# Optimization experiments

Hardware: AMD Instinct MI355X
Metric: run time of the kernel (lower is better)

## Reference

```python
import jax, jax.numpy as jnp
import numpy as np

VOCAB = 50000
EMB = 1024
HID = 1024
H = HID // 2            # per-direction hidden size
NTAG = 34
START = 32
STOP = 33
SEQ = 4096
NEG = -10000.0


def setup_inputs() -> dict:
    key = jax.random.key(0)
    ks = jax.random.split(key, 16)
    s = 0.05

    def rn(k, shape, scale=1.0):
        return (jax.random.normal(k, shape) * scale).astype(jnp.float32)

    logT = jax.random.normal(ks[12], (NTAG, NTAG)).astype(jnp.float32)
    logT = logT.at[START, :].set(NEG).at[:, STOP].set(NEG)
    return {
        "sentence": jax.random.randint(ks[0], (SEQ,), 0, VOCAB),
        "embed": rn(ks[1], (VOCAB, EMB), s),
        "w_ih_f": rn(ks[2], (4 * H, EMB), s), "w_hh_f": rn(ks[3], (4 * H, H), s),
        "b_ih_f": rn(ks[4], (4 * H,), s), "b_hh_f": rn(ks[5], (4 * H,), s),
        "w_ih_b": rn(ks[6], (4 * H, EMB), s), "w_hh_b": rn(ks[7], (4 * H, H), s),
        "b_ih_b": rn(ks[8], (4 * H,), s), "b_hh_b": rn(ks[9], (4 * H,), s),
        "W_out": rn(ks[10], (NTAG, HID), s), "b_out": rn(ks[11], (NTAG,), s),
        "log_transitions": logT,
        "h0": rn(ks[13], (2, H)),
        "c0": rn(ks[14], (2, H)),
    }


def _lstm(xg, w_hh, h0, c0):
    # xg: [S, 4H] precomputed input-side gate preactivations (incl. both biases)
    def step(carry, g_x):
        h, c = carry
        g = g_x + h @ w_hh.T
        i, f, gg, o = jnp.split(g, 4)          # torch gate order: i, f, g, o
        i = jax.nn.sigmoid(i)
        f = jax.nn.sigmoid(f)
        gg = jnp.tanh(gg)
        o = jax.nn.sigmoid(o)
        c = f * c + i * gg
        h = o * jnp.tanh(c)
        return (h, c), h
    _, hs = jax.lax.scan(step, (h0, c0), xg)
    return hs  # [S, H]


def reference(sentence, embed, w_ih_f, w_hh_f, b_ih_f, b_hh_f,
              w_ih_b, w_hh_b, b_ih_b, b_hh_b, W_out, b_out,
              log_transitions, h0, c0):
    x = embed[sentence]                                  # [S, EMB]
    # bidirectional LSTM, batch=1
    xg_f = x @ w_ih_f.T + (b_ih_f + b_hh_f)
    hs_f = _lstm(xg_f, w_hh_f, h0[0], c0[0])             # [S, H]
    xg_b = (x @ w_ih_b.T + (b_ih_b + b_hh_b))[::-1]
    hs_b = _lstm(xg_b, w_hh_b, h0[1], c0[1])[::-1]       # [S, H]
    feats = jnp.concatenate([hs_f, hs_b], -1) @ W_out.T + b_out  # [S, NTAG]

    # Viterbi decode (single fused scan instead of per-step host loop)
    init = jnp.full((NTAG,), NEG, jnp.float32).at[START].set(0.0)

    def vstep(fv, feat):
        scores = fv[None, :] + log_transitions           # [next, prev]
        bp = jnp.argmax(scores, axis=1)                  # backpointers
        return jnp.max(scores, axis=1) + feat, bp

    fv, bptrs = jax.lax.scan(vstep, init, feats)         # bptrs: [S, NTAG]
    terminal = fv + log_transitions[STOP]
    best = jnp.argmax(terminal)
    path_score = terminal[best]

    def btstep(tag, bp):
        return bp[tag], tag                              # emit tag at current t
    _, path_rev = jax.lax.scan(btstep, best, bptrs[::-1])
    best_path = path_rev[::-1]                           # [S] int tags
    return path_score, best_path
```

## Files before the change

### kernel.cpp

```cpp
#include <hip/hip_runtime.h>
#include <math.h>

#define SEQn 4096
#define EMBn 1024
#define Hn   512
#define G4n  2048
#define NTAGn 34
#define START_TAG 32
#define STOP_TAG 33
#define NEGV (-10000.0f)
#define NCHUNK 16
#define CHL 256
#define WARM 64
#define VCH 64
#define VCL 64
#define VWARM 128
#define PADNEG (-1.0e30f)

typedef unsigned long long ull;
typedef __attribute__((ext_vector_type(8))) short bf16x8;
typedef __attribute__((ext_vector_type(4))) float f32x4;
typedef __attribute__((ext_vector_type(2))) _Float16 half2v;

__device__ __forceinline__ unsigned f2bf(float f) {
  unsigned u = __float_as_uint(f);
  return (u + 0x7FFFu + ((u >> 16) & 1u)) >> 16;
}

__device__ __forceinline__ half2v pkh(float a, float b) {
  auto r = __builtin_amdgcn_cvt_pkrtz(a, b);
  return __builtin_bit_cast(half2v, r);
}

#if defined(__has_builtin)
#if __has_builtin(__builtin_amdgcn_fdot2)
#define HAS_FDOT2 1
#endif
#endif

__device__ __forceinline__ float dot2acc(half2v w, half2v h, float acc) {
#ifdef HAS_FDOT2
  return __builtin_amdgcn_fdot2(w, h, acc, false);
#else
  return acc + (float)w.x * (float)h.x + (float)w.y * (float)h.y;
#endif
}

__global__ __launch_bounds__(256) void xg_mfma_kernel(
    const int* __restrict__ sent, const float* __restrict__ embed,
    const float* __restrict__ w_f, const float* __restrict__ w_b,
    const float* __restrict__ bif, const float* __restrict__ bhf,
    const float* __restrict__ bib, const float* __restrict__ bhb,
    float* __restrict__ xgf, float* __restrict__ xgb)
{
  const int dz = blockIdx.z;
  const float* W   = dz ? w_b : w_f;
  const float* b1  = dz ? bib : bif;
  const float* b2  = dz ? bhb : bhf;
  float* C         = dz ? xgb : xgf;

  __shared__ unsigned short Alds[128 * 64];
  __shared__ unsigned short Blds[128 * 64];
  __shared__ int sent_s[128];

  const int tid = threadIdx.x;
  const int m0 = blockIdx.x * 128, n0 = blockIdx.y * 128;
  if (tid < 128) sent_s[tid] = sent[m0 + tid];

  const int w = tid >> 6, l = tid & 63;
  const int wm = w >> 1, wn = w & 1;

  const int srow = tid >> 4;
  const int scol = (tid & 15) * 4;

  f32x4 acc[4][4] = {};

  for (int kt = 0; kt < EMBn; kt += 64) {
    __syncthreads();
#pragma unroll
    for (int i = 0; i < 8; ++i) {
      int row = srow + i * 16;
      float4 va = *(const float4*)(embed + (size_t)sent_s[row] * EMBn + kt + scol);
      float4 vb = *(const float4*)(W + (size_t)(n0 + row) * EMBn + kt + scol);
      unsigned pa0 = f2bf(va.x) | (f2bf(va.y) << 16);
      unsigned pa1 = f2bf(va.z) | (f2bf(va.w) << 16);
      unsigned pb0 = f2bf(vb.x) | (f2bf(vb.y) << 16);
      unsigned pb1 = f2bf(vb.z) | (f2bf(vb.w) << 16);
      int idx = (row * 64 + scol) ^ ((row & 7) << 3);
      *(uint2*)&Alds[idx] = make_uint2(pa0, pa1);
      *(uint2*)&Blds[idx] = make_uint2(pb0, pb1);
    }
    __syncthreads();
#pragma unroll
    for (int kk = 0; kk < 2; ++kk) {
      bf16x8 af[4], bfr[4];
      const int kus = kk * 32 + (l >> 4) * 8;
#pragma unroll
      for (int mi = 0; mi < 4; ++mi) {
        int row = wm * 64 + mi * 16 + (l & 15);
        af[mi] = *(bf16x8*)&Alds[(row * 64 + kus) ^ ((row & 7) << 3)];
      }
#pragma unroll
      for (int ni = 0; ni < 4; ++ni) {
        int row = wn * 64 + ni * 16 + (l & 15);
        bfr[ni] = *(bf16x8*)&Blds[(row * 64 + kus) ^ ((row & 7) << 3)];
      }
#pragma unroll
      for (int mi = 0; mi < 4; ++mi)
#pragma unroll
        for (int ni = 0; ni < 4; ++ni)
          acc[mi][ni] = __builtin_amdgcn_mfma_f32_16x16x32_bf16(
              af[mi], bfr[ni], acc[mi][ni], 0, 0, 0);
    }
  }

  const int cm = m0 + wm * 64 + (l >> 4) * 4;
  const int cn = n0 + wn * 64 + (l & 15);
#pragma unroll
  for (int ni = 0; ni < 4; ++ni) {
    float bv = b1[cn + ni * 16] + b2[cn + ni * 16];
#pragma unroll
    for (int mi = 0; mi < 4; ++mi)
#pragma unroll
      for (int r = 0; r < 4; ++r)
        C[(size_t)(cm + mi * 16 + r) * G4n + cn + ni * 16] = acc[mi][ni][r] + bv;
  }
}

__global__ __launch_bounds__(1024) void lstm_kernel(
    const float* __restrict__ xg_f, const float* __restrict__ xg_b,
    const float* __restrict__ w_hh_f, const float* __restrict__ w_hh_b,
    const float* __restrict__ h0, const float* __restrict__ c0,
    float* __restrict__ hs, ull* __restrict__ hpair)
{
  const int bid = blockIdx.x;
  const int g = bid >> 3;
  const int blk = bid & 7;
  const int dir = g & 1;
  const int chunk = g >> 1;
  const int warm = chunk ? WARM : 0;
  const int nsteps = CHL + warm;
  const int s0 = dir ? (SEQn - 1 - chunk * CHL + warm) : (chunk * CHL - warm);

  const int hbase = blk * 64;
  const float* W  = dir ? w_hh_b : w_hh_f;
  const float* xg = dir ? xg_b : xg_f;
  ull* pairs = hpair + (size_t)g * 4 * Hn;

  const int t = threadIdx.x;
  const int w = t >> 6;
  const int l = t & 63;
  const bool isTW = (w == 2 * blk);

  half2v wreg[4][16];
#pragma unroll
  for (int q = 0; q < 4; ++q) {
    const float* wrow = W + (size_t)(q * Hn + hbase + l) * Hn + w * 32;
#pragma unroll
    for (int jj = 0; jj < 8; ++jj) {
      float4 v = *(const float4*)(wrow + jj * 4);
      wreg[q][2 * jj]     = pkh(v.x, v.y);
      wreg[q][2 * jj + 1] = pkh(v.z, v.w);
    }
  }

  __shared__ __align__(16) float h_lds[Hn];
  __shared__ float part[2][16 * 256];

  if (isTW) __builtin_amdgcn_s_setprio(1);

  float c_reg = 0.f;
  float xgc[4] = {}, xgn[4] = {};
  if (isTW) {
    if (chunk == 0) c_reg = c0[dir * Hn + hbase + l];
#pragma unroll
    for (int q = 0; q < 4; ++q)
      xgc[q] = xg[(size_t)s0 * G4n + q * Hn + hbase + l];
  }
  if (l < 32)
    h_lds[w * 32 + l] = (chunk == 0) ? h0[dir * Hn + w * 32 + l] : 0.f;

  for (int k = 0; k < nsteps; ++k) {
    const int par = k & 1;
    const int s = dir ? (s0 - k) : (s0 + k);

    if (isTW && (k + 1 < nsteps)) {
      const int s1 = dir ? (s0 - k - 1) : (s0 + k + 1);
#pragma unroll
      for (int q = 0; q < 4; ++q)
        xgn[q] = xg[(size_t)s1 * G4n + q * Hn + hbase + l];
    }

    if (!isTW && k > 0 && l < 32) {
      ull* p = pairs + (size_t)(k & 3) * Hn + w * 32 + l;
      ull v;
      do {
        v = __hip_atomic_load(p, __ATOMIC_RELAXED, __HIP_MEMORY_SCOPE_AGENT);
      } while ((unsigned)(v >> 32) != (unsigned)k);
      h_lds[w * 32 + l] = __uint_as_float((unsigned)v);
    }

    float a0 = 0.f, a1 = 0.f, a2 = 0.f, a3 = 0.f;
    {
      const float* hseg = h_lds + w * 32;
      half2v hp[16];
#pragma unroll
      for (int jj = 0; jj < 8; ++jj) {
        float4 hv = *(const float4*)(hseg + jj * 4);
        hp[2 * jj]     = pkh(hv.x, hv.y);
        hp[2 * jj + 1] = pkh(hv.z, hv.w);
      }
#pragma unroll
      for (int jj = 0; jj < 16; ++jj) {
        a0 = dot2acc(wreg[0][jj], hp[jj], a0);
        a1 = dot2acc(wreg[1][jj], hp[jj], a1);
        a2 = dot2acc(wreg[2][jj], hp[jj], a2);
        a3 = dot2acc(wreg[3][jj], hp[jj], a3);
      }
    }
    part[par][w * 256 + l]       = a0;
    part[par][w * 256 + 64 + l]  = a1;
    part[par][w * 256 + 128 + l] = a2;
    part[par][w * 256 + 192 + l] = a3;
    __syncthreads();

    if (isTW) {
      float g0 = xgc[0], g1 = xgc[1], g2 = xgc[2], g3 = xgc[3];
#pragma unroll
      for (int ww = 0; ww < 16; ++ww) {
        g0 += part[par][ww * 256 + l];
        g1 += part[par][ww * 256 + 64 + l];
        g2 += part[par][ww * 256 + 128 + l];
        g3 += part[par][ww * 256 + 192 + l];
      }
      float iv = 1.f / (1.f + __expf(-g0));
      float fv = 1.f / (1.f + __expf(-g1));
      float gg = 2.f / (1.f + __expf(-2.f * g2)) - 1.f;
      float ov = 1.f / (1.f + __expf(-g3));
      float c = fv * c_reg + iv * gg;
      c_reg = c;
      float e2 = __expf(-2.f * c);
      float h = ov * (1.f - e2) / (1.f + e2);

      if (k + 1 < nsteps) {
        ull pv = ((ull)(unsigned)(k + 1) << 32) | (ull)__float_as_uint(h);
        __hip_atomic_store(pairs + (size_t)((k + 1) & 3) * Hn + hbase + l, pv,
                           __ATOMIC_RELAXED, __HIP_MEMORY_SCOPE_AGENT);
      }
      if (l < 32) h_lds[hbase + l] = h;
      if (k >= warm)
        hs[(size_t)s * 1024 + dir * Hn + hbase + l] = h;
#pragma unroll
      for (int q = 0; q < 4; ++q) xgc[q] = xgn[q];
    }
  }
}

__global__ __launch_bounds__(64) void feats_kernel(
    const float* __restrict__ hs, const float* __restrict__ W_out,
    const float* __restrict__ b_out, float* __restrict__ feats)
{
  const int tq = blockIdx.x;
  const int lane = threadIdx.x;
  const float* hrow = hs + (size_t)tq * 1024;
  float4 hv[4];
#pragma unroll
  for (int i = 0; i < 4; ++i) hv[i] = *(const float4*)(hrow + lane * 16 + i * 4);

  for (int tag = 0; tag < NTAGn; ++tag) {
    const float* wrow = W_out + (size_t)tag * 1024 + lane * 16;
    float s = 0.f;
#pragma unroll
    for (int i = 0; i < 4; ++i) {
      float4 wv = *(const float4*)(wrow + i * 4);
      s += hv[i].x * wv.x + hv[i].y * wv.y + hv[i].z * wv.z + hv[i].w * wv.w;
    }
#pragma unroll
    for (int off = 32; off; off >>= 1) s += __shfl_xor(s, off);
    if (lane == 0) feats[(size_t)tq * NTAGn + tag] = s + b_out[tag];
  }
}

__global__ __launch_bounds__(64) void vit_chunk(
    const float* __restrict__ feats, const float* __restrict__ logT,
    unsigned char* __restrict__ pstore, int* __restrict__ Eg,
    float* __restrict__ fvfin)
{
  const int c = blockIdx.x;
  const int lane = threadIdx.x;
  const int start = c * VCL;
  const int wstart = (start - VWARM > 0) ? (start - VWARM) : 0;
  const int warm = start - wstart;
  const bool exact = (wstart == 0);
  const int nsteps = warm + VCL;

  __shared__ __align__(16) float fv_s[36];
  __shared__ unsigned char bpl[VCL][36];
  __shared__ __align__(16) float fl[VWARM + VCL][36];
  const bool active = lane < NTAGn;

  float Trow[36];
  if (active) {
#pragma unroll
    for (int j = 0; j < NTAGn; ++j) Trow[j] = logT[lane * NTAGn + j];
    Trow[34] = PADNEG; Trow[35] = PADNEG;
  }
  for (int x = lane; x < nsteps * NTAGn; x += 64) {
    int s = x / NTAGn, j = x - s * NTAGn;
    fl[s][j] = feats[(size_t)wstart * NTAGn + x];
  }
  if (lane < 36) {
    float init;
    if (exact) init = (lane == START_TAG) ? 0.f : ((lane < NTAGn) ? NEGV : PADNEG);
    else       init = (lane < NTAGn) ? 0.f : PADNEG;
    fv_s[lane] = init;
  }
  __syncthreads();

  for (int s = 0; s < nsteps; ++s) {
    float best = -3.4e38f; int bj = 0;
    if (active) {
      float sc[36];
#pragma unroll
      for (int q = 0; q < 9; ++q) {
        float4 f4 = *(const float4*)&fv_s[q * 4];
        sc[q*4+0] = f4.x + Trow[q*4+0];
        sc[q*4+1] = f4.y + Trow[q*4+1];
        sc[q*4+2] = f4.z + Trow[q*4+2];
        sc[q*4+3] = f4.w + Trow[q*4+3];
      }
      best = sc[0];
#pragma unroll
      for (int j = 1; j < 36; ++j) { if (sc[j] > best) { best = sc[j]; bj = j; } }
    }
    if (active) {
      fv_s[lane] = best + fl[s][lane];
      if (s >= warm) bpl[s - warm][lane] = (unsigned char)bj;
    }
    __threadfence_block();
  }
  __syncthreads();

  if (c == VCH - 1 && lane < 36) fvfin[lane] = fv_s[lane];

  if (active) {
    int p = lane;
    unsigned char* ps = pstore + ((size_t)c * NTAGn + lane) * VCL;
    for (int s = VCL - 1; s >= 1; --s) {
      ps[s] = (unsigned char)p;
      p = bpl[s][p];
    }
    ps[0] = (unsigned char)p;
    Eg[c * NTAGn + lane] = bpl[0][p];
  }
}

__global__ __launch_bounds__(64) void vit_final(
    const float* __restrict__ feats, const float* __restrict__ logT,
    const float* __restrict__ fvfin, const unsigned char* __restrict__ pstore,
    const int* __restrict__ Eg, float* __restrict__ out)
{
  const int lane = threadIdx.x;
  __shared__ float term[64];
  __shared__ int ec[VCH];
  __shared__ unsigned char path_lds[SEQn];

  term[lane] = (lane < NTAGn)
             ? (fvfin[lane] + logT[STOP_TAG * NTAGn + lane]) : -3.4e38f;
  __syncthreads();
  if (lane == 0) {
    float bv = -3.4e38f; int bi = 0;
#pragma unroll
    for (int i = 0; i < NTAGn; ++i) { if (term[i] > bv) { bv = term[i]; bi = i; } }
    int e = bi;
    for (int c = VCH - 1; c >= 1; --c) { ec[c] = e; e = Eg[c * NTAGn + e]; }
    ec[0] = e;
  }
  __syncthreads();
  for (int t = lane; t < SEQn; t += 64) {
    int c = t >> 6;
    unsigned char p = pstore[((size_t)c * NTAGn + ec[c]) * VCL + (t & 63)];
    path_lds[t] = p;
    out[1 + t] = (float)p;
  }
  __syncthreads();

  float s = 0.f;
  for (int t = lane; t < SEQn; t += 64) {
    int p = path_lds[t];
    int pp = (t == 0) ? START_TAG : (int)path_lds[t - 1];
    s += feats[(size_t)t * NTAGn + p] + logT[p * NTAGn + pp];
  }
#pragma unroll
  for (int off = 32; off; off >>= 1) s += __shfl_xor(s, off);
  if (lane == 0)
    out[0] = s + logT[STOP_TAG * NTAGn + (int)path_lds[SEQn - 1]];
}

extern "C" void kernel_launch(void* const* d_in, const int* in_sizes, int n_in,
                              void* d_out, int out_size, void* d_ws, size_t ws_size,
                              hipStream_t stream) {
  const int*   sent   = (const int*)d_in[0];
  const float* embed  = (const float*)d_in[1];
  const float* w_ih_f = (const float*)d_in[2];
  const float* w_hh_f = (const float*)d_in[3];
  const float* b_ih_f = (const float*)d_in[4];
  const float* b_hh_f = (const float*)d_in[5];
  const float* w_ih_b = (const float*)d_in[6];
  const float* w_hh_b = (const float*)d_in[7];
  const float* b_ih_b = (const float*)d_in[8];
  const float* b_hh_b = (const float*)d_in[9];
  const float* W_out  = (const float*)d_in[10];
  const float* b_out  = (const float*)d_in[11];
  const float* logT   = (const float*)d_in[12];
  const float* h0     = (const float*)d_in[13];
  const float* c0     = (const float*)d_in[14];
  float* out = (float*)d_out;

  char* ws = (char*)d_ws;
  size_t off = 0;
  float* xg_f  = (float*)(ws + off); off += (size_t)SEQn * G4n * 4;
  float* xg_b  = (float*)(ws + off); off += (size_t)SEQn * G4n * 4;
  float* hs    = (float*)(ws + off); off += (size_t)SEQn * 1024 * 4;
  float* feats = (float*)(ws + off); off += (size_t)SEQn * NTAGn * 4;
  ull*   hpair = (ull*)(ws + off);   off += (size_t)32 * 4 * Hn * 8;
  unsigned char* pstore = (unsigned char*)(ws + off); off += (size_t)VCH * NTAGn * VCL;
  int*   Eg    = (int*)(ws + off);   off += (size_t)VCH * NTAGn * 4;
  float* fvfin = (float*)(ws + off); off += 64 * 4;

  (void)hipMemsetAsync(hpair, 0, (size_t)32 * 4 * Hn * 8, stream);

  dim3 gg(SEQn / 128, G4n / 128, 2);
  xg_mfma_kernel<<<gg, 256, 0, stream>>>(sent, embed, w_ih_f, w_ih_b,
                                         b_ih_f, b_hh_f, b_ih_b, b_hh_b,
                                         xg_f, xg_b);

  lstm_kernel<<<256, 1024, 0, stream>>>(xg_f, xg_b, w_hh_f, w_hh_b, h0, c0,
                                        hs, hpair);

  feats_kernel<<<SEQn, 64, 0, stream>>>(hs, W_out, b_out, feats);

  vit_chunk<<<VCH, 64, 0, stream>>>(feats, logT, pstore, Eg, fvfin);
  vit_final<<<1, 64, 0, stream>>>(feats, logT, fvfin, pstore, Eg, out);
}
```

Before: 866.5 us.

## Use MFMA for output projection, unroll spin-wait polling, shorten LSTM warmup

Replaces the per-row wavefront dot-product feats kernel with a tiled bf16 MFMA GEMM that stages hs and W_out through swizzled LDS, so the 4096x1024x34 projection runs on matrix cores. The LSTM cross-block spin loop now issues four atomic loads per iteration, aiming to cut the latency of seeing the published h value. The chunked LSTM warmup length drops from 64 to 48 steps, which removes serial recurrence work. Rounding hs and W_out to bf16 and using a shorter warmup both change numerics and could alter the Viterbi path.

New measurement: 957.1 us. 10.5% more time.

```diff
diff --git a/kernel.cpp b/kernel.cpp
--- a/kernel.cpp
+++ b/kernel.cpp
@@ -11,7 +11,7 @@
 #define NEGV (-10000.0f)
 #define NCHUNK 16
 #define CHL 256
-#define WARM 64
+#define WARM 48
 #define VCH 64
 #define VCL 64
 #define VWARM 128
@@ -193,10 +193,18 @@
 
     if (!isTW && k > 0 && l < 32) {
       ull* p = pairs + (size_t)(k & 3) * Hn + w * 32 + l;
+      const unsigned want = (unsigned)k;
       ull v;
-      do {
-        v = __hip_atomic_load(p, __ATOMIC_RELAXED, __HIP_MEMORY_SCOPE_AGENT);
-      } while ((unsigned)(v >> 32) != (unsigned)k);
+      for (;;) {
+        ull v0 = __hip_atomic_load(p, __ATOMIC_RELAXED, __HIP_MEMORY_SCOPE_AGENT);
+        ull v1 = __hip_atomic_load(p, __ATOMIC_RELAXED, __HIP_MEMORY_SCOPE_AGENT);
+        ull v2 = __hip_atomic_load(p, __ATOMIC_RELAXED, __HIP_MEMORY_SCOPE_AGENT);
+        ull v3 = __hip_atomic_load(p, __ATOMIC_RELAXED, __HIP_MEMORY_SCOPE_AGENT);
+        if ((unsigned)(v0 >> 32) == want) { v = v0; break; }
+        if ((unsigned)(v1 >> 32) == want) { v = v1; break; }
+        if ((unsigned)(v2 >> 32) == want) { v = v2; break; }
+        if ((unsigned)(v3 >> 32) == want) { v = v3; break; }
+      }
       h_lds[w * 32 + l] = __uint_as_float((unsigned)v);
     }
 
@@ -256,28 +264,82 @@
   }
 }
 
-__global__ __launch_bounds__(64) void feats_kernel(
+__global__ __launch_bounds__(256) void feats_mfma_kernel(
     const float* __restrict__ hs, const float* __restrict__ W_out,
     const float* __restrict__ b_out, float* __restrict__ feats)
 {
-  const int tq = blockIdx.x;
-  const int lane = threadIdx.x;
-  const float* hrow = hs + (size_t)tq * 1024;
-  float4 hv[4];
-#pragma unroll
-  for (int i = 0; i < 4; ++i) hv[i] = *(const float4*)(hrow + lane * 16 + i * 4);
-
-  for (int tag = 0; tag < NTAGn; ++tag) {
-    const float* wrow = W_out + (size_t)tag * 1024 + lane * 16;
-    float s = 0.f;
-#pragma unroll
-    for (int i = 0; i < 4; ++i) {
-      float4 wv = *(const float4*)(wrow + i * 4);
-      s += hv[i].x * wv.x + hv[i].y * wv.y + hv[i].z * wv.z + hv[i].w * wv.w;
-    }
-#pragma unroll
-    for (int off = 32; off; off >>= 1) s += __shfl_xor(s, off);
-    if (lane == 0) feats[(size_t)tq * NTAGn + tag] = s + b_out[tag];
+  __shared__ unsigned short Alds[128 * 64];
+  __shared__ unsigned short Blds[48 * 64];
+
+  const int tid = threadIdx.x;
+  const int m0 = blockIdx.x * 128;
+  const int w = tid >> 6, l = tid & 63;
+
+  const int srow = tid >> 4;
+  const int scol = (tid & 15) * 4;
+
+  f32x4 acc[2][3] = {};
+
+  for (int kt = 0; kt < 1024; kt += 64) {
+    __syncthreads();
+#pragma unroll
+    for (int i = 0; i < 8; ++i) {
+      int row = srow + i * 16;
+      float4 va = *(const float4*)(hs + (size_t)(m0 + row) * 1024 + kt + scol);
+      unsigned pa0 = f2bf(va.x) | (f2bf(va.y) << 16);
+      unsigned pa1 = f2bf(va.z) | (f2bf(va.w) << 16);
+      int idx = (row * 64 + scol) ^ ((row & 7) << 3);
+      *(uint2*)&Alds[idx] = make_uint2(pa0, pa1);
+    }
+#pragma unroll
+    for (int i = 0; i < 3; ++i) {
+      int row = srow + i * 16;
+      uint2 pb = make_uint2(0u, 0u);
+      if (row < NTAGn) {
+        float4 vb = *(const float4*)(W_out + (size_t)row * 1024 + kt + scol);
+        pb.x = f2bf(vb.x) | (f2bf(vb.y) << 16);
+        pb.y = f2bf(vb.z) | (f2bf(vb.w) << 16);
+      }
+      int idx = (row * 64 + scol) ^ ((row & 7) << 3);
+      *(uint2*)&Blds[idx] = pb;
+    }
+    __syncthreads();
+#pragma unroll
+    for (int kk = 0; kk < 2; ++kk) {
+      const int kus = kk * 32 + (l >> 4) * 8;
+      bf16x8 af[2], bfr[3];
+#pragma unroll
+      for (int mi = 0; mi < 2; ++mi) {
+        int row = w * 32 + mi * 16 + (l & 15);
+        af[mi] = *(bf16x8*)&Alds[(row * 64 + kus) ^ ((row & 7) << 3)];
+      }
+#pragma unroll
+      for (int ni = 0; ni < 3; ++ni) {
+        int row = ni * 16 + (l & 15);
+        bfr[ni] = *(bf16x8*)&Blds[(row * 64 + kus) ^ ((row & 7) << 3)];
+      }
+#pragma unroll
+      for (int mi = 0; mi < 2; ++mi)
+#pragma unroll
+        for (int ni = 0; ni < 3; ++ni)
+          acc[mi][ni] = __builtin_amdgcn_mfma_f32_16x16x32_bf16(
+              af[mi], bfr[ni], acc[mi][ni], 0, 0, 0);
+    }
+  }
+
+  const int cm = m0 + w * 32 + (l >> 4) * 4;
+  const int cn = l & 15;
+#pragma unroll
+  for (int ni = 0; ni < 3; ++ni) {
+    int col = cn + ni * 16;
+    if (col < NTAGn) {
+      float bv = b_out[col];
+#pragma unroll
+      for (int mi = 0; mi < 2; ++mi)
+#pragma unroll
+        for (int r = 0; r < 4; ++r)
+          feats[(size_t)(cm + mi * 16 + r) * NTAGn + col] = acc[mi][ni][r] + bv;
+    }
   }
 }
 
@@ -438,7 +500,7 @@
   lstm_kernel<<<256, 1024, 0, stream>>>(xg_f, xg_b, w_hh_f, w_hh_b, h0, c0,
                                         hs, hpair);
 
-  feats_kernel<<<SEQn, 64, 0, stream>>>(hs, W_out, b_out, feats);
+  feats_mfma_kernel<<<SEQn / 128, 256, 0, stream>>>(hs, W_out, b_out, feats);
 
   vit_chunk<<<VCH, 64, 0, stream>>>(feats, logT, pstore, Eg, fvfin);
   vit_final<<<1, 64, 0, stream>>>(feats, logT, fvfin, pstore, Eg, out);
```
